# Optimization experiments

Measured on AMD Instinct MI355X. Metric: run time of the kernel, lower is better.

## Reference

```python
import jax, jax.numpy as jnp
import numpy as np

VOCAB = 2_000_000
NUM_TAGS = 32
SEQ_LEN = 16384
START = 0  # tag2id['<s>']
END = 1    # tag2id['</s>']


def setup_inputs() -> dict:
    key = jax.random.key(0)
    k1, k2, k3 = jax.random.split(key, 3)
    x = jax.random.randint(k1, (SEQ_LEN,), 0, VOCAB)
    emit_score = jax.random.normal(k2, (VOCAB, NUM_TAGS), dtype=jnp.float32)
    transitions = jax.random.normal(k3, (NUM_TAGS, NUM_TAGS), dtype=jnp.float32)
    # same masking as the torch __init__
    transitions = transitions.at[:, START].set(-10000.0)
    transitions = transitions.at[END, :].set(-10000.0)
    return {"x": x, "emit_score": emit_score, "transitions": transitions}


def reference(x, emit_score, transitions):
    """CRF forward algorithm (log partition function Z), fused via lax.scan."""
    num_tags = transitions.shape[0]
    init_alphas = jnp.full((num_tags,), -10000.0, dtype=transitions.dtype)
    init_alphas = init_alphas.at[START].set(0.0)

    emits = emit_score[x]  # [L, T] gather (memory-bound)

    def step(alphas, emit_t):
        # score[i, j] = alphas[i] + transitions[i, j] + emit_t[j]
        score = alphas[:, None] + transitions + emit_t[None, :]
        new_alphas = jax.nn.logsumexp(score, axis=0)  # stable log-sum-exp over prev tag
        return new_alphas, None

    alphas, _ = jax.lax.scan(step, init_alphas, emits)
    alphas = alphas + transitions[:, END]
    z = jax.nn.logsumexp(alphas)  # scalar log partition
    return z
```

## Files before the change

kernel.cpp:

```cpp
#include <hip/hip_runtime.h>

#define LOG2E_F 1.44269504088896340736f
#define LN2_F   0.69314718055994530942f

static constexpr int NT     = 32;
static constexpr int SEQ    = 16384;
static constexpr int LC     = 64;
static constexpr int CHUNKS = SEQ / LC;
static constexpr int GROUP  = 8;
static constexpr int NB2    = CHUNKS / GROUP;

__device__ __forceinline__ float redmax32(float v) {
    #pragma unroll
    for (int m = 16; m >= 1; m >>= 1) v = fmaxf(v, __shfl_xor(v, m, 32));
    return v;
}
__device__ __forceinline__ float redsum32(float v) {
    #pragma unroll
    for (int m = 16; m >= 1; m >>= 1) v += __shfl_xor(v, m, 32);
    return v;
}

__global__ __launch_bounds__(1024, 4)
void crf_phase1(const int* __restrict__ x,
                const float* __restrict__ emit,
                const float* __restrict__ trans,
                float* __restrict__ out1)
{
    __shared__ float W[NT * NT];
    __shared__ float P[2][NT * NT];
    __shared__ float E[LC * NT];

    const int tid = threadIdx.x;
    const int i   = tid >> 5;
    const int k   = tid & 31;
    const int c   = blockIdx.x;
    const int base = c * LC;

    W[tid] = exp2f(trans[tid] * LOG2E_F);

    #pragma unroll
    for (int r = 0; r < 2; ++r) {
        const int row = (tid >> 5) + 32 * r;
        const int xv  = x[base + row];
        E[row * NT + k] = exp2f(emit[(size_t)xv * NT + k] * LOG2E_F);
    }
    __syncthreads();

    float wcol[NT];
    #pragma unroll
    for (int j = 0; j < NT; ++j) wcol[j] = W[j * NT + k];

    float tmp = W[i * NT + k] * E[k];
    int sInt = 0;
    P[0][tid] = tmp;
    __syncthreads();

    int p = 0;
    for (int t = 1; t < LC; ++t) {
        const float4* prow = (const float4*)&P[p][i * NT];
        float acc = 0.f;
        #pragma unroll
        for (int q = 0; q < 8; ++q) {
            float4 v = prow[q];
            acc += v.x * wcol[4 * q + 0];
            acc += v.y * wcol[4 * q + 1];
            acc += v.z * wcol[4 * q + 2];
            acc += v.w * wcol[4 * q + 3];
        }
        acc *= E[t * NT + k];

        float rm = redmax32(acc);
        int ex = 0;
        if (rm > 0.f) ex = (int)((__float_as_uint(rm) >> 23) & 0xFF) - 127;
        tmp = ldexpf(acc, -ex);
        sInt += ex;

        P[p ^ 1][tid] = tmp;
        p ^= 1;
        __syncthreads();
    }
    out1[c * (NT * NT) + tid] = (float)sInt + log2f(tmp);
}

__global__ __launch_bounds__(1024, 4)
void crf_phase2a(const float* __restrict__ out1, float* __restrict__ out2)
{
    __shared__ float D[2][NT * NT];
    __shared__ float Lb[NT * NT];

    const int tid = threadIdx.x;
    const int i = tid >> 5, k = tid & 31;
    const int b = blockIdx.x;

    float dcur = out1[(b * GROUP) * (NT * NT) + tid];
    D[0][tid] = dcur;
    int p = 0;
    for (int n = 1; n < GROUP; ++n) {
        Lb[tid] = out1[(b * GROUP + n) * (NT * NT) + tid];
        __syncthreads();

        const float4* drow = (const float4*)&D[p][i * NT];
        float vals[NT];
        #pragma unroll
        for (int q = 0; q < 8; ++q) {
            float4 v = drow[q];
            vals[4 * q + 0] = v.x + Lb[(4 * q + 0) * NT + k];
            vals[4 * q + 1] = v.y + Lb[(4 * q + 1) * NT + k];
            vals[4 * q + 2] = v.z + Lb[(4 * q + 2) * NT + k];
            vals[4 * q + 3] = v.w + Lb[(4 * q + 3) * NT + k];
        }
        float m = vals[0];
        #pragma unroll
        for (int j = 1; j < NT; ++j) m = fmaxf(m, vals[j]);
        m = fmaxf(m, -3.0e38f);
        float s = 0.f;
        #pragma unroll
        for (int j = 0; j < NT; ++j) s += exp2f(vals[j] - m);
        dcur = (s > 0.f) ? (m + log2f(s)) : -__builtin_inff();

        __syncthreads();
        D[p ^ 1][tid] = dcur;
        p ^= 1;
    }
    out2[b * (NT * NT) + tid] = dcur;
}

__global__ __launch_bounds__(1024, 2)
void crf_phase2b(const float* __restrict__ out2,
                 const float* __restrict__ trans,
                 float* __restrict__ out)
{
    __shared__ float Lt[GROUP][NT * 33];
    __shared__ float la[NT];

    const int tid = threadIdx.x;
    const int k = tid >> 5;
    const int i = tid & 31;

    if (tid < NT) la[tid] = (tid == 0) ? 0.f : -10000.f * LOG2E_F;

    for (int g = 0; g < NB2 / GROUP; ++g) {
        __syncthreads();
        {
            const int i2 = tid >> 5, k2 = tid & 31;
            #pragma unroll
            for (int n = 0; n < GROUP; ++n) {
                float v = out2[(g * GROUP + n) * (NT * NT) + tid];
                Lt[n][k2 * 33 + i2] = v;
            }
        }
        __syncthreads();
        for (int n = 0; n < GROUP; ++n) {
            float val = la[i] + Lt[n][k * 33 + i];
            float m = redmax32(val);
            m = fmaxf(m, -3.0e38f);
            float s = redsum32(exp2f(val - m));
            __syncthreads();
            if (i == 0) la[k] = (s > 0.f) ? (m + log2f(s)) : -__builtin_inff();
            __syncthreads();
        }
    }

    if (tid < NT) {
        float v = la[tid] + trans[tid * NT + 1] * LOG2E_F;
        float m = redmax32(v);
        m = fmaxf(m, -3.0e38f);
        float s = redsum32(exp2f(v - m));
        if (tid == 0) out[0] = (m + log2f(s)) * LN2_F;
    }
}

extern "C" void kernel_launch(void* const* d_in, const int* in_sizes, int n_in,
                              void* d_out, int out_size, void* d_ws, size_t ws_size,
                              hipStream_t stream) {
    const int*   x     = (const int*)d_in[0];
    const float* emit  = (const float*)d_in[1];
    const float* trans = (const float*)d_in[2];
    float* out = (float*)d_out;

    float* ws1 = (float*)d_ws;
    float* ws2 = ws1 + CHUNKS * NT * NT;

    crf_phase1 <<<CHUNKS, 1024, 0, stream>>>(x, emit, trans, ws1);
    crf_phase2a<<<NB2,    1024, 0, stream>>>(ws1, ws2);
    crf_phase2b<<<1,      1024, 0, stream>>>(ws2, trans, out);
}
```

Baseline: 363.8 us.

## Rewrite CRF chunk scan with single-wave bf16 MFMA matrix products

All three kernels are rewritten to use one 64-lane wave per block instead of 1024 threads. The per-chunk transfer-matrix products and the group reductions become bf16 MFMA 32x32x16 multiplies, with results redistributed between steps by register shuffles instead of shared memory and block barriers. Renormalisation in phase 1 runs every four steps, the group size grows to 16, and a per-chunk scale is stored separately. The aim is to remove barrier and shared-memory latency from the serial dependency chains, at the cost of bf16 precision in the probability-space products.

```diff
diff --git a/kernel.cpp b/kernel.cpp
--- a/kernel.cpp
+++ b/kernel.cpp
@@ -1,174 +1,280 @@
 #include <hip/hip_runtime.h>
 
-#define LOG2E_F 1.44269504088896340736f
-#define LN2_F   0.69314718055994530942f
+#define LOG2E 1.44269504088896340736f
+#define LN2   0.69314718055994530942f
 
 static constexpr int NT     = 32;
 static constexpr int SEQ    = 16384;
 static constexpr int LC     = 64;
 static constexpr int CHUNKS = SEQ / LC;
-static constexpr int GROUP  = 8;
+static constexpr int GROUP  = 16;
 static constexpr int NB2    = CHUNKS / GROUP;
 
-__device__ __forceinline__ float redmax32(float v) {
-    #pragma unroll
-    for (int m = 16; m >= 1; m >>= 1) v = fmaxf(v, __shfl_xor(v, m, 32));
+typedef __attribute__((ext_vector_type(8)))  short short8;
+typedef __attribute__((ext_vector_type(16))) float float16_t;
+
+union U8 { unsigned u[4]; short8 s; };
+
+__device__ __forceinline__ unsigned pack_bf16(float a, float b) {
+    unsigned ua = (__float_as_uint(a) + 0x8000u) >> 16;
+    unsigned ub = (__float_as_uint(b) + 0x8000u) & 0xFFFF0000u;
+    return ua | ub;
+}
+
+__device__ __forceinline__ float wave_max(float v) {
+    #pragma unroll
+    for (int m = 1; m <= 32; m <<= 1) v = fmaxf(v, __shfl_xor(v, m, 64));
     return v;
 }
-__device__ __forceinline__ float redsum32(float v) {
-    #pragma unroll
-    for (int m = 16; m >= 1; m >>= 1) v += __shfl_xor(v, m, 32);
-    return v;
-}
-
-__global__ __launch_bounds__(1024, 4)
-void crf_phase1(const int* __restrict__ x,
-                const float* __restrict__ emit,
+
+#define PACK_SWAP_TO_B(ACC, B0, B1)                                          \
+    {                                                                        \
+        unsigned P0 = pack_bf16(ACC[0],  ACC[1]);                            \
+        unsigned P1 = pack_bf16(ACC[2],  ACC[3]);                            \
+        unsigned P2 = pack_bf16(ACC[4],  ACC[5]);                            \
+        unsigned P3 = pack_bf16(ACC[6],  ACC[7]);                            \
+        unsigned P4 = pack_bf16(ACC[8],  ACC[9]);                            \
+        unsigned P5 = pack_bf16(ACC[10], ACC[11]);                           \
+        unsigned P6 = pack_bf16(ACC[12], ACC[13]);                           \
+        unsigned P7 = pack_bf16(ACC[14], ACC[15]);                           \
+        unsigned q0 = __shfl_xor(P0, 32, 64), q1 = __shfl_xor(P1, 32, 64);   \
+        unsigned q2 = __shfl_xor(P2, 32, 64), q3 = __shfl_xor(P3, 32, 64);   \
+        unsigned q4 = __shfl_xor(P4, 32, 64), q5 = __shfl_xor(P5, 32, 64);   \
+        unsigned q6 = __shfl_xor(P6, 32, 64), q7 = __shfl_xor(P7, 32, 64);   \
+        B0.u[0] = hi ? q2 : P0; B0.u[1] = hi ? q3 : P1;                      \
+        B0.u[2] = hi ? P2 : q0; B0.u[3] = hi ? P3 : q1;                      \
+        B1.u[0] = hi ? q6 : P4; B1.u[1] = hi ? q7 : P5;                      \
+        B1.u[2] = hi ? P6 : q4; B1.u[3] = hi ? P7 : q5;                      \
+    }
+
+#define IDENTITY_B(B0, B1)                                                   \
+    {                                                                        \
+        _Pragma("unroll")                                                    \
+        for (int q = 0; q < 4; ++q) {                                        \
+            unsigned lo = ((8*h + 2*q)     == c) ? 0x3F80u : 0u;             \
+            unsigned hb = ((8*h + 2*q + 1) == c) ? 0x3F80u : 0u;             \
+            B0.u[q] = lo | (hb << 16);                                       \
+            lo = ((16 + 8*h + 2*q)     == c) ? 0x3F80u : 0u;                 \
+            hb = ((16 + 8*h + 2*q + 1) == c) ? 0x3F80u : 0u;                 \
+            B1.u[q] = lo | (hb << 16);                                       \
+        }                                                                    \
+    }
+
+__global__ __launch_bounds__(64, 1)
+void crf_phase1(const int* __restrict__ x, const float* __restrict__ emit,
                 const float* __restrict__ trans,
-                float* __restrict__ out1)
+                float* __restrict__ out1, float* __restrict__ out1S)
 {
-    __shared__ float W[NT * NT];
-    __shared__ float P[2][NT * NT];
-    __shared__ float E[LC * NT];
-
-    const int tid = threadIdx.x;
-    const int i   = tid >> 5;
-    const int k   = tid & 31;
-    const int c   = blockIdx.x;
-    const int base = c * LC;
-
-    W[tid] = exp2f(trans[tid] * LOG2E_F);
-
-    #pragma unroll
-    for (int r = 0; r < 2; ++r) {
-        const int row = (tid >> 5) + 32 * r;
-        const int xv  = x[base + row];
-        E[row * NT + k] = exp2f(emit[(size_t)xv * NT + k] * LOG2E_F);
+    __shared__ __align__(16) float E[LC * NT];
+    const int L = threadIdx.x;
+    const int c = L & 31;
+    const int h = L >> 5;
+    const bool hi = (h != 0);
+    const int chunk = blockIdx.x;
+
+    int xv = x[chunk * LC + L];
+    float ev[32];
+    #pragma unroll
+    for (int rr = 0; rr < 32; ++rr) {
+        int t = 2 * rr + h;
+        int xt = __shfl(xv, t, 64);
+        ev[rr] = emit[(size_t)xt * NT + c];
+    }
+    #pragma unroll
+    for (int rr = 0; rr < 32; ++rr) {
+        int t = 2 * rr + h;
+        E[t * NT + c] = exp2f(ev[rr] * LOG2E);
     }
     __syncthreads();
 
-    float wcol[NT];
-    #pragma unroll
-    for (int j = 0; j < NT; ++j) wcol[j] = W[j * NT + k];
-
-    float tmp = W[i * NT + k] * E[k];
+    U8 A0, A1;
+    #pragma unroll
+    for (int q = 0; q < 4; ++q) {
+        float w0 = exp2f(trans[(8*h + 2*q    ) * NT + c] * LOG2E);
+        float w1 = exp2f(trans[(8*h + 2*q + 1) * NT + c] * LOG2E);
+        A0.u[q] = pack_bf16(w0, w1);
+        float w2 = exp2f(trans[(16 + 8*h + 2*q    ) * NT + c] * LOG2E);
+        float w3 = exp2f(trans[(16 + 8*h + 2*q + 1) * NT + c] * LOG2E);
+        A1.u[q] = pack_bf16(w2, w3);
+    }
+
+    U8 B0, B1;
+    IDENTITY_B(B0, B1);
+
     int sInt = 0;
-    P[0][tid] = tmp;
+    float16_t acc;
+    for (int t = 0; t < LC; ++t) {
+        float16_t z = {};
+        acc = __builtin_amdgcn_mfma_f32_32x32x16_bf16(A0.s, B0.s, z,   0, 0, 0);
+        acc = __builtin_amdgcn_mfma_f32_32x32x16_bf16(A1.s, B1.s, acc, 0, 0, 0);
+
+        const float* Et = &E[t * NT + 4 * h];
+        float4 e0 = *(const float4*)(Et);
+        float4 e1 = *(const float4*)(Et + 8);
+        float4 e2 = *(const float4*)(Et + 16);
+        float4 e3 = *(const float4*)(Et + 24);
+        acc[0]  *= e0.x; acc[1]  *= e0.y; acc[2]  *= e0.z; acc[3]  *= e0.w;
+        acc[4]  *= e1.x; acc[5]  *= e1.y; acc[6]  *= e1.z; acc[7]  *= e1.w;
+        acc[8]  *= e2.x; acc[9]  *= e2.y; acc[10] *= e2.z; acc[11] *= e2.w;
+        acc[12] *= e3.x; acc[13] *= e3.y; acc[14] *= e3.z; acc[15] *= e3.w;
+
+        if ((t & 3) == 3) {
+            float mx = acc[0];
+            #pragma unroll
+            for (int i = 1; i < 16; ++i) mx = fmaxf(mx, acc[i]);
+            mx = wave_max(mx);
+            if (mx >= 1.1754944e-38f) {
+                int ex = (int)((__float_as_uint(mx) >> 23) & 255) - 127;
+                #pragma unroll
+                for (int i = 0; i < 16; ++i) acc[i] = ldexpf(acc[i], -ex);
+                sInt += ex;
+            }
+        }
+        PACK_SWAP_TO_B(acc, B0, B1);
+    }
+
+    float mx = acc[0];
+    #pragma unroll
+    for (int i = 1; i < 16; ++i) mx = fmaxf(mx, acc[i]);
+    mx = wave_max(mx);
+    float lm = log2f(mx);
+    float* o = out1 + (size_t)chunk * (NT * NT);
+    #pragma unroll
+    for (int i = 0; i < 16; ++i) {
+        int r = 4 * h + (i & 3) + 8 * (i >> 2);
+        o[r * NT + c] = log2f(acc[i]) - lm;
+    }
+    if (L == 0) out1S[chunk] = (float)sInt + lm;
+}
+
+__global__ __launch_bounds__(64, 1)
+void crf_phase2a(const float* __restrict__ out1, const float* __restrict__ out1S,
+                 float* __restrict__ out2)
+{
+    const int L = threadIdx.x;
+    const int c = L & 31;
+    const int h = L >> 5;
+    const bool hi = (h != 0);
+    const int w = blockIdx.x;
+
+    U8 B0, B1;
+    IDENTITY_B(B0, B1);
+
+    float SC = 0.f;
+    #pragma unroll
+    for (int n = 0; n < GROUP; ++n) SC += out1S[w * GROUP + n];
+
+    const float* src = out1 + (size_t)(w * GROUP) * (NT * NT) + c * NT + 8 * h;
+    float4 a0 = *(const float4*)(src);
+    float4 a1 = *(const float4*)(src + 4);
+    float4 a2 = *(const float4*)(src + 16);
+    float4 a3 = *(const float4*)(src + 20);
+
+    int sInt = 0;
+    float16_t acc;
+    for (int n = 0; n < GROUP; ++n) {
+        U8 A0, A1;
+        A0.u[0] = pack_bf16(exp2f(a0.x), exp2f(a0.y));
+        A0.u[1] = pack_bf16(exp2f(a0.z), exp2f(a0.w));
+        A0.u[2] = pack_bf16(exp2f(a1.x), exp2f(a1.y));
+        A0.u[3] = pack_bf16(exp2f(a1.z), exp2f(a1.w));
+        A1.u[0] = pack_bf16(exp2f(a2.x), exp2f(a2.y));
+        A1.u[1] = pack_bf16(exp2f(a2.z), exp2f(a2.w));
+        A1.u[2] = pack_bf16(exp2f(a3.x), exp2f(a3.y));
+        A1.u[3] = pack_bf16(exp2f(a3.z), exp2f(a3.w));
+
+        if (n + 1 < GROUP) {
+            const float* s2 = out1 + (size_t)(w * GROUP + n + 1) * (NT * NT)
+                              + c * NT + 8 * h;
+            a0 = *(const float4*)(s2);
+            a1 = *(const float4*)(s2 + 4);
+            a2 = *(const float4*)(s2 + 16);
+            a3 = *(const float4*)(s2 + 20);
+        }
+
+        float16_t z = {};
+        acc = __builtin_amdgcn_mfma_f32_32x32x16_bf16(A0.s, B0.s, z,   0, 0, 0);
+        acc = __builtin_amdgcn_mfma_f32_32x32x16_bf16(A1.s, B1.s, acc, 0, 0, 0);
+
+        float mx = acc[0];
+        #pragma unroll
+        for (int i = 1; i < 16; ++i) mx = fmaxf(mx, acc[i]);
+        mx = wave_max(mx);
+        if (mx >= 1.1754944e-38f) {
+            int ex = (int)((__float_as_uint(mx) >> 23) & 255) - 127;
+            #pragma unroll
+            for (int i = 0; i < 16; ++i) acc[i] = ldexpf(acc[i], -ex);
+            sInt += ex;
+        }
+        PACK_SWAP_TO_B(acc, B0, B1);
+    }
+
+    float* o = out2 + (size_t)w * (NT * NT);
+    float addc = (float)sInt + SC;
+    #pragma unroll
+    for (int i = 0; i < 16; ++i) {
+        int r = 4 * h + (i & 3) + 8 * (i >> 2);
+        o[r * NT + c] = log2f(acc[i]) + addc;
+    }
+}
+
+__global__ __launch_bounds__(64, 1)
+void crf_phase2b(const float* __restrict__ out2, const float* __restrict__ trans,
+                 float* __restrict__ out)
+{
+    __shared__ __align__(16) float al[NT];
+    const int L = threadIdx.x;
+    const int r = L & 31;
+    const int h = L >> 5;
+
+    if (L < NT) al[L] = (L == 0) ? 0.f : -10000.f * LOG2E;
     __syncthreads();
 
-    int p = 0;
-    for (int t = 1; t < LC; ++t) {
-        const float4* prow = (const float4*)&P[p][i * NT];
-        float acc = 0.f;
+    const float* src = out2 + r * NT + 16 * h;
+    float4 v0 = *(const float4*)(src);
+    float4 v1 = *(const float4*)(src + 4);
+    float4 v2 = *(const float4*)(src + 8);
+    float4 v3 = *(const float4*)(src + 12);
+
+    for (int n = 0; n < NB2; ++n) {
+        float vals[16] = {v0.x, v0.y, v0.z, v0.w, v1.x, v1.y, v1.z, v1.w,
+                          v2.x, v2.y, v2.z, v2.w, v3.x, v3.y, v3.z, v3.w};
+        if (n + 1 < NB2) {
+            const float* s2 = out2 + (size_t)(n + 1) * (NT * NT) + r * NT + 16 * h;
+            v0 = *(const float4*)(s2);
+            v1 = *(const float4*)(s2 + 4);
+            v2 = *(const float4*)(s2 + 8);
+            v3 = *(const float4*)(s2 + 12);
+        }
+        const float4* ap = (const float4*)&al[16 * h];
+        float4 A0 = ap[0], A1 = ap[1], A2 = ap[2], A3 = ap[3];
+        float aj[16] = {A0.x, A0.y, A0.z, A0.w, A1.x, A1.y, A1.z, A1.w,
+                        A2.x, A2.y, A2.z, A2.w, A3.x, A3.y, A3.z, A3.w};
+        float mv = -3.0e38f;
         #pragma unroll
-        for (int q = 0; q < 8; ++q) {
-            float4 v = prow[q];
-            acc += v.x * wcol[4 * q + 0];
-            acc += v.y * wcol[4 * q + 1];
-            acc += v.z * wcol[4 * q + 2];
-            acc += v.w * wcol[4 * q + 3];
-        }
-        acc *= E[t * NT + k];
-
-        float rm = redmax32(acc);
-        int ex = 0;
-        if (rm > 0.f) ex = (int)((__float_as_uint(rm) >> 23) & 0xFF) - 127;
-        tmp = ldexpf(acc, -ex);
-        sInt += ex;
-
-        P[p ^ 1][tid] = tmp;
-        p ^= 1;
-        __syncthreads();
-    }
-    out1[c * (NT * NT) + tid] = (float)sInt + log2f(tmp);
-}
-
-__global__ __launch_bounds__(1024, 4)
-void crf_phase2a(const float* __restrict__ out1, float* __restrict__ out2)
-{
-    __shared__ float D[2][NT * NT];
-    __shared__ float Lb[NT * NT];
-
-    const int tid = threadIdx.x;
-    const int i = tid >> 5, k = tid & 31;
-    const int b = blockIdx.x;
-
-    float dcur = out1[(b * GROUP) * (NT * NT) + tid];
-    D[0][tid] = dcur;
-    int p = 0;
-    for (int n = 1; n < GROUP; ++n) {
-        Lb[tid] = out1[(b * GROUP + n) * (NT * NT) + tid];
-        __syncthreads();
-
-        const float4* drow = (const float4*)&D[p][i * NT];
-        float vals[NT];
-        #pragma unroll
-        for (int q = 0; q < 8; ++q) {
-            float4 v = drow[q];
-            vals[4 * q + 0] = v.x + Lb[(4 * q + 0) * NT + k];
-            vals[4 * q + 1] = v.y + Lb[(4 * q + 1) * NT + k];
-            vals[4 * q + 2] = v.z + Lb[(4 * q + 2) * NT + k];
-            vals[4 * q + 3] = v.w + Lb[(4 * q + 3) * NT + k];
-        }
-        float m = vals[0];
-        #pragma unroll
-        for (int j = 1; j < NT; ++j) m = fmaxf(m, vals[j]);
-        m = fmaxf(m, -3.0e38f);
+        for (int j = 0; j < 16; ++j) {
+            vals[j] = fmaxf(vals[j], -1e30f) + fmaxf(aj[j], -1e30f);
+            mv = fmaxf(mv, vals[j]);
+        }
+        mv = fmaxf(mv, __shfl_xor(mv, 32, 64));
         float s = 0.f;
         #pragma unroll
-        for (int j = 0; j < NT; ++j) s += exp2f(vals[j] - m);
-        dcur = (s > 0.f) ? (m + log2f(s)) : -__builtin_inff();
-
+        for (int j = 0; j < 16; ++j) s += exp2f(vals[j] - mv);
+        s += __shfl_xor(s, 32, 64);
+        float nal = mv + log2f(s);
         __syncthreads();
-        D[p ^ 1][tid] = dcur;
-        p ^= 1;
-    }
-    out2[b * (NT * NT) + tid] = dcur;
-}
-
-__global__ __launch_bounds__(1024, 2)
-void crf_phase2b(const float* __restrict__ out2,
-                 const float* __restrict__ trans,
-                 float* __restrict__ out)
-{
-    __shared__ float Lt[GROUP][NT * 33];
-    __shared__ float la[NT];
-
-    const int tid = threadIdx.x;
-    const int k = tid >> 5;
-    const int i = tid & 31;
-
-    if (tid < NT) la[tid] = (tid == 0) ? 0.f : -10000.f * LOG2E_F;
-
-    for (int g = 0; g < NB2 / GROUP; ++g) {
+        if (h == 0) al[r] = nal;
         __syncthreads();
-        {
-            const int i2 = tid >> 5, k2 = tid & 31;
-            #pragma unroll
-            for (int n = 0; n < GROUP; ++n) {
-                float v = out2[(g * GROUP + n) * (NT * NT) + tid];
-                Lt[n][k2 * 33 + i2] = v;
-            }
-        }
-        __syncthreads();
-        for (int n = 0; n < GROUP; ++n) {
-            float val = la[i] + Lt[n][k * 33 + i];
-            float m = redmax32(val);
-            m = fmaxf(m, -3.0e38f);
-            float s = redsum32(exp2f(val - m));
-            __syncthreads();
-            if (i == 0) la[k] = (s > 0.f) ? (m + log2f(s)) : -__builtin_inff();
-            __syncthreads();
-        }
-    }
-
-    if (tid < NT) {
-        float v = la[tid] + trans[tid * NT + 1] * LOG2E_F;
-        float m = redmax32(v);
-        m = fmaxf(m, -3.0e38f);
-        float s = redsum32(exp2f(v - m));
-        if (tid == 0) out[0] = (m + log2f(s)) * LN2_F;
-    }
+    }
+
+    float v = fmaxf(al[r], -1e30f) + trans[r * NT + 1] * LOG2E;
+    float mv = v;
+    #pragma unroll
+    for (int m = 1; m <= 16; m <<= 1) mv = fmaxf(mv, __shfl_xor(mv, m, 64));
+    float s = exp2f(v - mv);
+    #pragma unroll
+    for (int m = 1; m <= 16; m <<= 1) s += __shfl_xor(s, m, 64);
+    if (L == 0) out[0] = (mv + log2f(s)) * LN2;
 }
 
 extern "C" void kernel_launch(void* const* d_in, const int* in_sizes, int n_in,
@@ -179,10 +285,11 @@
     const float* trans = (const float*)d_in[2];
     float* out = (float*)d_out;
 
-    float* ws1 = (float*)d_ws;
-    float* ws2 = ws1 + CHUNKS * NT * NT;
-
-    crf_phase1 <<<CHUNKS, 1024, 0, stream>>>(x, emit, trans, ws1);
-    crf_phase2a<<<NB2,    1024, 0, stream>>>(ws1, ws2);
-    crf_phase2b<<<1,      1024, 0, stream>>>(ws2, trans, out);
-}
+    float* ws1   = (float*)d_ws;
+    float* ws2   = ws1 + (size_t)CHUNKS * NT * NT;
+    float* ws1S  = ws2 + (size_t)NB2 * NT * NT;
+
+    crf_phase1 <<<CHUNKS, 64, 0, stream>>>(x, emit, trans, ws1, ws1S);
+    crf_phase2a<<<NB2,    64, 0, stream>>>(ws1, ws1S, ws2);
+    crf_phase2b<<<1,      64, 0, stream>>>(ws2, trans, out);
+}
```

Result: faster. 328.1 us (-9.8%).
